# Kernel tuning notes

Hardware: AMD Instinct MI355X
Metric: run time of the kernel (lower is better)

The kernel has to match this reference:

```python
import jax, jax.numpy as jnp
import numpy as np

BS, SEQ, DIM, NH = 4, 2048, 768, 12
DH = DIM // NH  # 64


def setup_inputs() -> dict:
    key = jax.random.key(0)
    ks = jax.random.split(key, 12)
    s = 1.0 / np.sqrt(DIM)
    return {
        "query": jax.random.normal(ks[0], (BS, SEQ, DIM), jnp.float32),
        "key_": jax.random.normal(ks[1], (BS, SEQ, DIM), jnp.float32),
        "value": jax.random.normal(ks[2], (BS, SEQ, DIM), jnp.float32),
        "mask": jax.random.randint(ks[3], (BS, SEQ), 0, 2, jnp.int32),
        "q_w": jax.random.uniform(ks[4], (DIM, DIM), jnp.float32, -s, s),
        "q_b": jax.random.uniform(ks[5], (DIM,), jnp.float32, -s, s),
        "k_w": jax.random.uniform(ks[6], (DIM, DIM), jnp.float32, -s, s),
        "k_b": jax.random.uniform(ks[7], (DIM,), jnp.float32, -s, s),
        "v_w": jax.random.uniform(ks[8], (DIM, DIM), jnp.float32, -s, s),
        "v_b": jax.random.uniform(ks[9], (DIM,), jnp.float32, -s, s),
        "o_w": jax.random.uniform(ks[10], (DIM, DIM), jnp.float32, -s, s),
        "o_b": jax.random.uniform(ks[11], (DIM,), jnp.float32, -s, s),
    }


def reference(query, key_, value, mask, q_w, q_b, k_w, k_b, v_w, v_b, o_w, o_b):
    bs, q_len, _ = query.shape
    # linear projections (torch Linear: x @ W.T + b), split heads -> [b, h, s, d]
    def shape(x):
        return x.reshape(bs, -1, NH, DH).transpose(0, 2, 1, 3)

    q = shape(query @ q_w.T + q_b) / jnp.sqrt(jnp.asarray(DH, query.dtype))
    k = shape(key_ @ k_w.T + k_b)
    v = shape(value @ v_w.T + v_b)

    scores = jnp.einsum("bhqd,bhkd->bhqk", q, k)  # [b, h, q, k]
    neg = jnp.finfo(scores.dtype).min
    pad = (mask == 0)[:, None, None, :]  # [b,1,1,k]
    scores = jnp.where(pad, neg, scores)
    weights = jax.nn.softmax(scores, axis=-1)
    # dropout is identity in eval / deterministic reference
    context = jnp.einsum("bhqk,bhkd->bhqd", weights, v)
    context = context.transpose(0, 2, 1, 3).reshape(bs, q_len, DIM)
    return context @ o_w.T + o_b
```

## Files before the change

### kernel.cpp

```cpp
#include <hip/hip_runtime.h>
#include <hip/hip_bf16.h>

typedef __attribute__((ext_vector_type(8))) short short8;
typedef __attribute__((ext_vector_type(4))) float f32x4;
typedef __attribute__((ext_vector_type(4))) unsigned short u16x4;
typedef __attribute__((ext_vector_type(4))) int int4v;
typedef __attribute__((ext_vector_type(2))) unsigned int u32x2;

#define DEVI static __device__ __forceinline__

constexpr int B_ = 4, S_ = 2048, D_ = 768, NH_ = 12, DH_ = 64;
constexpr int M_ = B_ * S_;
constexpr size_t NX = (size_t)M_ * D_;
constexpr size_t NW = (size_t)D_ * D_;

DEVI unsigned short f2bf(float f) {
  union { float f; unsigned u; } c; c.f = f;
  unsigned u = c.u;
  return (unsigned short)((u + 0x7FFFu + ((u >> 16) & 1u)) >> 16);
}

DEVI unsigned cvtpk_bf16(float lo, float hi) {
  unsigned r;
  asm("v_cvt_pk_bf16_f32 %0, %1, %2" : "=v"(r) : "v"(lo), "v"(hi));
  return r;
}

DEVI float fexp2(float x) {
  float r;
  asm("v_exp_f32 %0, %1" : "=v"(r) : "v"(x));
  return r;
}

DEVI void gload16(const void* g, void* l) {
  __builtin_amdgcn_global_load_lds(
      (const __attribute__((address_space(1))) void*)g,
      (__attribute__((address_space(3))) void*)l, 16, 0, 0);
}

__global__ __launch_bounds__(256) void convert_kernel(
    const float* __restrict__ q, const float* __restrict__ k,
    const float* __restrict__ v, const float* __restrict__ qw_,
    const float* __restrict__ kw_, const float* __restrict__ vw_,
    const float* __restrict__ ow_, const int* __restrict__ smask,
    unsigned short* __restrict__ Xq, unsigned short* __restrict__ Xk,
    unsigned short* __restrict__ Xv, unsigned short* __restrict__ Wc,
    float* __restrict__ dmask) {
  const long bid = blockIdx.x;
  const int tid = threadIdx.x;
  if (bid < 18432) {
    const int seg = (int)(bid / 6144);
    const long i = (bid % 6144) * 256 + tid;
    const float* src = seg == 0 ? q : seg == 1 ? k : v;
    unsigned short* dst = seg == 0 ? Xq : seg == 1 ? Xk : Xv;
    f32x4 vv = *(const f32x4*)(src + i * 4);
    u16x4 o;
    o.x = f2bf(vv.x); o.y = f2bf(vv.y); o.z = f2bf(vv.z); o.w = f2bf(vv.w);
    *(u16x4*)(dst + i * 4) = o;
  } else if (bid < 20736) {
    const long e = ((bid - 18432) * 256 + tid) * 4;
    const int j = (int)(e / (long)NW);
    const float* src = j == 0 ? qw_ : j == 1 ? kw_ : j == 2 ? vw_ : ow_;
    f32x4 vv = *(const f32x4*)(src + (e - (long)j * NW));
    u16x4 o;
    o.x = f2bf(vv.x); o.y = f2bf(vv.y); o.z = f2bf(vv.z); o.w = f2bf(vv.w);
    *(u16x4*)(Wc + e) = o;
  } else {
    const long i = (bid - 20736) * 256 + tid;
    int4v m = *(const int4v*)(smask + i * 4);
    f32x4 o;
    o.x = m.x ? -4.0f : -1e30f; o.y = m.y ? -4.0f : -1e30f;
    o.z = m.z ? -4.0f : -1e30f; o.w = m.w ? -4.0f : -1e30f;
    *(f32x4*)(dmask + i * 4) = o;
  }
}

DEVI void gemm_core(const unsigned short* __restrict__ A,
                    const unsigned short* __restrict__ Bt,
                    unsigned short* As, unsigned short* Bs,
                    int m0, int n0, int tid, f32x4 acc[4][4]) {
  const int w = tid >> 6, l = tid & 63;
  const int wm = w >> 1, wn = w & 1;
  const int lr = l & 15, lg = l >> 4;

  const unsigned short* gA0 = A  + (size_t)(m0 + (tid >> 2)) * 768 + (tid & 3) * 8;
  const unsigned short* gB0 = Bt + (size_t)(n0 + (tid >> 2)) * 768 + (tid & 3) * 8;
  const int wslot = w * 512;

  gload16(gA0, As + wslot);
  gload16(gA0 + (size_t)64 * 768, As + wslot + 2048);
  gload16(gB0, Bs + wslot);
  gload16(gB0 + (size_t)64 * 768, Bs + wslot + 2048);

  int buf = 0;
  for (int k0 = 0; k0 < 768; k0 += 32) {
    if (k0 + 32 < 768) {
      const int nb = (buf ^ 1) * 4096;
      gload16(gA0 + k0 + 32, As + nb + wslot);
      gload16(gA0 + (size_t)64 * 768 + k0 + 32, As + nb + wslot + 2048);
      gload16(gB0 + k0 + 32, Bs + nb + wslot);
      gload16(gB0 + (size_t)64 * 768 + k0 + 32, Bs + nb + wslot + 2048);
      asm volatile("s_waitcnt vmcnt(4)" ::: "memory");
    } else {
      asm volatile("s_waitcnt vmcnt(0)" ::: "memory");
    }
    __builtin_amdgcn_s_barrier();

    const unsigned short* fA = As + buf * 4096 + (size_t)(wm * 64 + lr) * 32 + lg * 8;
    const unsigned short* fB = Bs + buf * 4096 + (size_t)(wn * 64 + lr) * 32 + lg * 8;
    short8 af[4], bf[4];
#pragma unroll
    for (int m = 0; m < 4; m++) af[m] = *(const short8*)(fA + m * 16 * 32);
#pragma unroll
    for (int n = 0; n < 4; n++) bf[n] = *(const short8*)(fB + n * 16 * 32);
    __builtin_amdgcn_s_setprio(1);
#pragma unroll
    for (int m = 0; m < 4; m++)
#pragma unroll
      for (int n = 0; n < 4; n++)
        acc[m][n] = __builtin_amdgcn_mfma_f32_16x16x32_bf16(af[m], bf[n], acc[m][n], 0, 0, 0);
    __builtin_amdgcn_s_setprio(0);
    __builtin_amdgcn_s_barrier();
    buf ^= 1;
  }
}

__global__ __launch_bounds__(256) void qkv_gemm(
    const unsigned short* __restrict__ Xq, const unsigned short* __restrict__ Xk,
    const unsigned short* __restrict__ Xv,
    const unsigned short* __restrict__ Wq, const unsigned short* __restrict__ Wk,
    const unsigned short* __restrict__ Wv,
    const float* __restrict__ bq, const float* __restrict__ bk,
    const float* __restrict__ bv,
    unsigned short* __restrict__ Oq, unsigned short* __restrict__ Ok,
    unsigned short* __restrict__ Vt) {
  __shared__ unsigned short SH[16384];
  const int z = blockIdx.z;
  const unsigned short* A  = (z == 0) ? Xq : (z == 1) ? Xk : Xv;
  const unsigned short* Bt = (z == 0) ? Wq : (z == 1) ? Wk : Wv;
  const float* bias        = (z == 0) ? bq : (z == 1) ? bk : bv;
  const float scale = (z == 0) ? 0.125f * 1.44269504f : 1.0f;

  const int m0 = blockIdx.x * 128, n0 = blockIdx.y * 128;
  f32x4 acc[4][4] = {};
  gemm_core(A, Bt, SH, SH + 8192, m0, n0, threadIdx.x, acc);

  const int tid = threadIdx.x, w = tid >> 6, l = tid & 63;
  const int wm = w >> 1, wn = w & 1, lr = l & 15, lg = l >> 4;
  if (z == 2) {
#pragma unroll
    for (int n = 0; n < 4; n++) {
      const int row = wn * 64 + n * 16 + lr;
      const float bvv = bias[n0 + row];
#pragma unroll
      for (int m = 0; m < 4; m++) {
        const int colb = wm * 64 + m * 16 + lg * 4;
        u16x4 v4;
#pragma unroll
        for (int r = 0; r < 4; r++) v4[r] = f2bf(acc[m][n][r] + bvv);
        *(u16x4*)&SH[row * 128 + (colb ^ ((row & 15) << 3))] = v4;
      }
    }
    __syncthreads();
    const int brow = m0 >> 11;
    const int s0 = m0 & 2047;
    const int u = tid & 15;
#pragma unroll
    for (int p = 0; p < 8; p++) {
      const int row = (tid >> 4) + 16 * p;
      short8 v = *(const short8*)&SH[row * 128 + ((u ^ (row & 15)) << 3)];
      const int ng = n0 + row;
      const int h = ng >> 6, d = ng & 63;
      *(short8*)&Vt[((size_t)(brow * NH_ + h) * DH_ + d) * S_ + s0 + u * 8] = v;
    }
  } else {
    unsigned short* O = (z == 0) ? Oq : Ok;
#pragma unroll
    for (int n = 0; n < 4; n++) {
      const int ng = n0 + wn * 64 + n * 16 + lr;
      const float bvv = bias[ng];
      const int h = ng >> 6, d = ng & 63;
#pragma unroll
      for (int m = 0; m < 4; m++) {
#pragma unroll
        for (int r = 0; r < 4; r++) {
          const int mg = m0 + wm * 64 + m * 16 + lg * 4 + r;
          const int b = mg >> 11, s = mg & 2047;
          O[((size_t)(b * NH_ + h) * S_ + s) * DH_ + d] = f2bf((acc[m][n][r] + bvv) * scale);
        }
      }
    }
  }
}

__global__ __launch_bounds__(256) void out_gemm(
    const unsigned short* __restrict__ A, const unsigned short* __restrict__ Bt,
    const float* __restrict__ bias, float* __restrict__ out) {
  __shared__ unsigned short As[2 * 4096], Bs[2 * 4096];
  const int m0 = blockIdx.x * 128, n0 = blockIdx.y * 128;
  f32x4 acc[4][4] = {};
  gemm_core(A, Bt, As, Bs, m0, n0, threadIdx.x, acc);

  const int tid = threadIdx.x, w = tid >> 6, l = tid & 63;
  const int wm = w >> 1, wn = w & 1, lr = l & 15, lg = l >> 4;
#pragma unroll
  for (int n = 0; n < 4; n++) {
    const int ng = n0 + wn * 64 + n * 16 + lr;
    const float bvv = bias[ng];
#pragma unroll
    for (int m = 0; m < 4; m++) {
#pragma unroll
      for (int r = 0; r < 4; r++) {
        const int mg = m0 + wm * 64 + m * 16 + lg * 4 + r;
        out[(size_t)mg * 768 + ng] = acc[m][n][r] + bvv;
      }
    }
  }
}

__global__ __launch_bounds__(512, 6) void attn_kernel(
    const unsigned short* __restrict__ Qp, const unsigned short* __restrict__ Kp,
    const unsigned short* __restrict__ Vt, const float* __restrict__ maskadd,
    unsigned short* __restrict__ Ctx) {
  __shared__ unsigned short KsA[4096], KsB[4096];
  __shared__ unsigned short VsA[4096], VsB[4096];

  const int id = blockIdx.x;
  const int xcd = id & 7, slot = id >> 3;
  const int bh = xcd + 8 * (slot >> 4);
  const int qt = slot & 15;
  const int b = bh / NH_, h = bh % NH_;
  const int tid = threadIdx.x, w = tid >> 6, l = tid & 63;
  const int lr = l & 15, lg = l >> 4;
  const int rsw = lr & 7;
  const int qw = qt * 128 + w * 16;

  const unsigned short* Qb = Qp + ((size_t)bh * S_ + qw + lr) * DH_ + lg * 8;
  const short8 aq0 = *(const short8*)(Qb);
  const short8 aq1 = *(const short8*)(Qb + 32);

  const int r0 = tid >> 3, c0 = tid & 7;
  const int cg = c0 ^ (r0 & 7);
  const unsigned short* Kg0 = Kp + ((size_t)bh * S_ + r0) * DH_ + cg * 8;
  const unsigned short* Vg0 = Vt + ((size_t)bh * DH_ + r0) * S_ + cg * 8;
  const int wslot = w * 512;

  const float* Mb = maskadd + b * S_ + lg * 4;

  float l_run = 0.f;
  f32x4 ctx[4] = {};

  unsigned short *Krd = KsA, *Vrd = VsA, *Kwr = KsB, *Vwr = VsB;

  gload16(Kg0, KsA + wslot);
  gload16(Vg0, VsA + wslot);
  f32x4 mkc[4];
#pragma unroll
  for (int t = 0; t < 4; t++) mkc[t] = *(const f32x4*)(Mb + 16 * t);
  __syncthreads();

  for (int kt = 0; kt < S_ / 64; kt++) {
    if (kt + 1 < S_ / 64) {
      gload16(Kg0 + (size_t)(kt + 1) * 64 * DH_, Kwr + wslot);
      gload16(Vg0 + (kt + 1) * 64, Vwr + wslot);
    }

    f32x4 sacc[4];
#pragma unroll
    for (int t = 0; t < 4; t++) sacc[t] = mkc[t];
    if (kt + 1 < S_ / 64) {
      const int kvn = (kt + 1) * 64;
#pragma unroll
      for (int t = 0; t < 4; t++) mkc[t] = *(const f32x4*)(Mb + kvn + 16 * t);
    }

    __builtin_amdgcn_s_setprio(1);
#pragma unroll
    for (int t = 0; t < 4; t++) {
      const int row = 16 * t + lr;
      short8 kf0 = *(const short8*)&Krd[row * 64 + ((lg) ^ rsw) * 8];
      short8 kf1 = *(const short8*)&Krd[row * 64 + ((lg + 4) ^ rsw) * 8];
      sacc[t] = __builtin_amdgcn_mfma_f32_16x16x32_bf16(kf0, aq0, sacc[t], 0, 0, 0);
      sacc[t] = __builtin_amdgcn_mfma_f32_16x16x32_bf16(kf1, aq1, sacc[t], 0, 0, 0);
    }
    __builtin_amdgcn_s_setprio(0);

    float ts = 0.f;
#pragma unroll
    for (int t = 0; t < 4; t++)
#pragma unroll
      for (int r = 0; r < 4; r++) {
        const float p = fexp2(sacc[t][r]);
        sacc[t][r] = p; ts += p;
      }
    ts += __shfl_xor(ts, 16);
    ts += __shfl_xor(ts, 32);
    l_run += ts;

    short8 pa[2];
#pragma unroll
    for (int half = 0; half < 2; half++) {
      const int t0 = 2 * half;
      unsigned Ax = cvtpk_bf16(sacc[t0][0], sacc[t0][1]);
      unsigned Ay = cvtpk_bf16(sacc[t0][2], sacc[t0][3]);
      unsigned Bx = cvtpk_bf16(sacc[t0 + 1][0], sacc[t0 + 1][1]);
      unsigned By = cvtpk_bf16(sacc[t0 + 1][2], sacc[t0 + 1][3]);
      asm("v_permlane32_swap_b32 %0, %1" : "+v"(Ax), "+v"(Bx));
      asm("v_permlane16_swap_b32 %0, %1" : "+v"(Ax), "+v"(Bx));
      asm("v_permlane32_swap_b32 %0, %1" : "+v"(Ay), "+v"(By));
      asm("v_permlane16_swap_b32 %0, %1" : "+v"(Ay), "+v"(By));
      union { unsigned u4[4]; short8 s8; } pk;
      pk.u4[0] = Ax; pk.u4[1] = Ay; pk.u4[2] = Bx; pk.u4[3] = By;
      pa[half] = pk.s8;
    }

    __builtin_amdgcn_s_setprio(1);
#pragma unroll
    for (int dt = 0; dt < 4; dt++) {
      const int row = 16 * dt + lr;
      short8 vf0 = *(const short8*)&Vrd[row * 64 + ((lg) ^ rsw) * 8];
      short8 vf1 = *(const short8*)&Vrd[row * 64 + ((lg + 4) ^ rsw) * 8];
      ctx[dt] = __builtin_amdgcn_mfma_f32_16x16x32_bf16(pa[0], vf0, ctx[dt], 0, 0, 0);
      ctx[dt] = __builtin_amdgcn_mfma_f32_16x16x32_bf16(pa[1], vf1, ctx[dt], 0, 0, 0);
    }
    __builtin_amdgcn_s_setprio(0);

    __syncthreads();
    unsigned short* t0p = Krd; Krd = Kwr; Kwr = t0p;
    unsigned short* t1p = Vrd; Vrd = Vwr; Vwr = t1p;
  }

  const float linv = 1.f / l_run;
  float iv[4];
#pragma unroll
  for (int r = 0; r < 4; r++) iv[r] = __shfl(linv, lg * 4 + r, 16);
#pragma unroll
  for (int r = 0; r < 4; r++) {
    const int qg = qw + lg * 4 + r;
#pragma unroll
    for (int dt = 0; dt < 4; dt++) {
      Ctx[((size_t)b * S_ + qg) * D_ + h * DH_ + dt * 16 + lr] =
          f2bf(ctx[dt][r] * iv[r]);
    }
  }
}

extern "C" void kernel_launch(void* const* d_in, const int* in_sizes, int n_in,
                              void* d_out, int out_size, void* d_ws, size_t ws_size,
                              hipStream_t stream) {
  const float* q   = (const float*)d_in[0];
  const float* k   = (const float*)d_in[1];
  const float* v   = (const float*)d_in[2];
  const int* mask  = (const int*)d_in[3];
  const float* q_w = (const float*)d_in[4];
  const float* q_b = (const float*)d_in[5];
  const float* k_w = (const float*)d_in[6];
  const float* k_b = (const float*)d_in[7];
  const float* v_w = (const float*)d_in[8];
  const float* v_b = (const float*)d_in[9];
  const float* o_w = (const float*)d_in[10];
  const float* o_b = (const float*)d_in[11];
  float* out = (float*)d_out;

  unsigned short* ws = (unsigned short*)d_ws;
  unsigned short* Xq = ws;
  unsigned short* Xk = Xq + NX;
  unsigned short* Xv = Xk + NX;
  unsigned short* Wq = Xv + NX;
  unsigned short* Wk = Wq + NW;
  unsigned short* Wv = Wk + NW;
  unsigned short* Wo = Wv + NW;
  unsigned short* Qp = Wo + NW;
  unsigned short* Kp = Qp + NX;
  unsigned short* Vt = Kp + NX;
  float* Ma = (float*)(Vt + NX);
  unsigned short* Ctx = Xq;

  convert_kernel<<<dim3(20744), dim3(256), 0, stream>>>(
      q, k, v, q_w, k_w, v_w, o_w, mask, Xq, Xk, Xv, Wq, Ma);

  qkv_gemm<<<dim3(64, 6, 3), dim3(256), 0, stream>>>(
      Xq, Xk, Xv, Wq, Wk, Wv, q_b, k_b, v_b, Qp, Kp, Vt);

  attn_kernel<<<dim3(768), dim3(512), 0, stream>>>(Qp, Kp, Vt, Ma, Ctx);

  out_gemm<<<dim3(64, 6), dim3(256), 0, stream>>>(Ctx, Wo, o_b, out);
}
```

Baseline: 156.4 us.

## Process two 16-row query blocks per wave to reuse K/V fragments

Each wave in the attention kernel now handles 32 query rows (two 16-row blocks) instead of 16, so each query tile covers 256 rows and the grid halves to 384 blocks. Every K and V fragment read from LDS feeds twice as many MFMAs, and K/V global traffic per query is halved. The cost is more registers per thread: launch bounds drop from 6 to 4 waves, and 384 blocks on 256 CUs may leave work unevenly spread across CUs.

Result: slower. 165.4 us (+5.8%).

```diff
diff --git a/kernel.cpp b/kernel.cpp
--- a/kernel.cpp
+++ b/kernel.cpp
@@ -218,7 +218,7 @@
   }
 }
 
-__global__ __launch_bounds__(512, 6) void attn_kernel(
+__global__ __launch_bounds__(512, 4) void attn_kernel(
     const unsigned short* __restrict__ Qp, const unsigned short* __restrict__ Kp,
     const unsigned short* __restrict__ Vt, const float* __restrict__ maskadd,
     unsigned short* __restrict__ Ctx) {
@@ -227,17 +227,21 @@
 
   const int id = blockIdx.x;
   const int xcd = id & 7, slot = id >> 3;
-  const int bh = xcd + 8 * (slot >> 4);
-  const int qt = slot & 15;
+  const int bh = xcd + 8 * (slot >> 3);
+  const int qt = slot & 7;
   const int b = bh / NH_, h = bh % NH_;
   const int tid = threadIdx.x, w = tid >> 6, l = tid & 63;
   const int lr = l & 15, lg = l >> 4;
   const int rsw = lr & 7;
-  const int qw = qt * 128 + w * 16;
-
-  const unsigned short* Qb = Qp + ((size_t)bh * S_ + qw + lr) * DH_ + lg * 8;
-  const short8 aq0 = *(const short8*)(Qb);
-  const short8 aq1 = *(const short8*)(Qb + 32);
+  const int qw = qt * 256 + w * 32;
+
+  short8 aq[2][2];
+#pragma unroll
+  for (int qb = 0; qb < 2; qb++)
+#pragma unroll
+    for (int ks = 0; ks < 2; ks++)
+      aq[qb][ks] = *(const short8*)&Qp[((size_t)bh * S_ + qw + qb * 16 + lr) * DH_ +
+                                       lg * 8 + ks * 32];
 
   const int r0 = tid >> 3, c0 = tid & 7;
   const int cg = c0 ^ (r0 & 7);
@@ -247,8 +251,8 @@
 
   const float* Mb = maskadd + b * S_ + lg * 4;
 
-  float l_run = 0.f;
-  f32x4 ctx[4] = {};
+  float l_run[2] = {0.f, 0.f};
+  f32x4 ctx[2][4] = {};
 
   unsigned short *Krd = KsA, *Vrd = VsA, *Kwr = KsB, *Vwr = VsB;
 
@@ -265,53 +269,56 @@
       gload16(Vg0 + (kt + 1) * 64, Vwr + wslot);
     }
 
-    f32x4 sacc[4];
-#pragma unroll
-    for (int t = 0; t < 4; t++) sacc[t] = mkc[t];
-    if (kt + 1 < S_ / 64) {
-      const int kvn = (kt + 1) * 64;
-#pragma unroll
-      for (int t = 0; t < 4; t++) mkc[t] = *(const f32x4*)(Mb + kvn + 16 * t);
-    }
-
+    f32x4 sacc[2][4];
     __builtin_amdgcn_s_setprio(1);
 #pragma unroll
     for (int t = 0; t < 4; t++) {
       const int row = 16 * t + lr;
       short8 kf0 = *(const short8*)&Krd[row * 64 + ((lg) ^ rsw) * 8];
       short8 kf1 = *(const short8*)&Krd[row * 64 + ((lg + 4) ^ rsw) * 8];
-      sacc[t] = __builtin_amdgcn_mfma_f32_16x16x32_bf16(kf0, aq0, sacc[t], 0, 0, 0);
-      sacc[t] = __builtin_amdgcn_mfma_f32_16x16x32_bf16(kf1, aq1, sacc[t], 0, 0, 0);
+      sacc[0][t] = __builtin_amdgcn_mfma_f32_16x16x32_bf16(kf0, aq[0][0], mkc[t], 0, 0, 0);
+      sacc[0][t] = __builtin_amdgcn_mfma_f32_16x16x32_bf16(kf1, aq[0][1], sacc[0][t], 0, 0, 0);
+      sacc[1][t] = __builtin_amdgcn_mfma_f32_16x16x32_bf16(kf0, aq[1][0], mkc[t], 0, 0, 0);
+      sacc[1][t] = __builtin_amdgcn_mfma_f32_16x16x32_bf16(kf1, aq[1][1], sacc[1][t], 0, 0, 0);
     }
     __builtin_amdgcn_s_setprio(0);
 
-    float ts = 0.f;
-#pragma unroll
-    for (int t = 0; t < 4; t++)
-#pragma unroll
-      for (int r = 0; r < 4; r++) {
-        const float p = fexp2(sacc[t][r]);
-        sacc[t][r] = p; ts += p;
+    if (kt + 1 < S_ / 64) {
+      const int kvn = (kt + 1) * 64;
+#pragma unroll
+      for (int t = 0; t < 4; t++) mkc[t] = *(const f32x4*)(Mb + kvn + 16 * t);
+    }
+
+    short8 pa[2][2];
+#pragma unroll
+    for (int qb = 0; qb < 2; qb++) {
+      float ts = 0.f;
+#pragma unroll
+      for (int t = 0; t < 4; t++)
+#pragma unroll
+        for (int r = 0; r < 4; r++) {
+          const float p = fexp2(sacc[qb][t][r]);
+          sacc[qb][t][r] = p; ts += p;
+        }
+      ts += __shfl_xor(ts, 16);
+      ts += __shfl_xor(ts, 32);
+      l_run[qb] += ts;
+
+#pragma unroll
+      for (int half = 0; half < 2; half++) {
+        const int t0 = 2 * half;
+        unsigned Ax = cvtpk_bf16(sacc[qb][t0][0], sacc[qb][t0][1]);
+        unsigned Ay = cvtpk_bf16(sacc[qb][t0][2], sacc[qb][t0][3]);
+        unsigned Bx = cvtpk_bf16(sacc[qb][t0 + 1][0], sacc[qb][t0 + 1][1]);
+        unsigned By = cvtpk_bf16(sacc[qb][t0 + 1][2], sacc[qb][t0 + 1][3]);
+        asm("v_permlane32_swap_b32 %0, %1" : "+v"(Ax), "+v"(Bx));
+        asm("v_permlane16_swap_b32 %0, %1" : "+v"(Ax), "+v"(Bx));
+        asm("v_permlane32_swap_b32 %0, %1" : "+v"(Ay), "+v"(By));
+        asm("v_permlane16_swap_b32 %0, %1" : "+v"(Ay), "+v"(By));
+        union { unsigned u4[4]; short8 s8; } pk;
+        pk.u4[0] = Ax; pk.u4[1] = Ay; pk.u4[2] = Bx; pk.u4[3] = By;
+        pa[qb][half] = pk.s8;
       }
-    ts += __shfl_xor(ts, 16);
-    ts += __shfl_xor(ts, 32);
-    l_run += ts;
-
-    short8 pa[2];
-#pragma unroll
-    for (int half = 0; half < 2; half++) {
-      const int t0 = 2 * half;
-      unsigned Ax = cvtpk_bf16(sacc[t0][0], sacc[t0][1]);
-      unsigned Ay = cvtpk_bf16(sacc[t0][2], sacc[t0][3]);
-      unsigned Bx = cvtpk_bf16(sacc[t0 + 1][0], sacc[t0 + 1][1]);
-      unsigned By = cvtpk_bf16(sacc[t0 + 1][2], sacc[t0 + 1][3]);
-      asm("v_permlane32_swap_b32 %0, %1" : "+v"(Ax), "+v"(Bx));
-      asm("v_permlane16_swap_b32 %0, %1" : "+v"(Ax), "+v"(Bx));
-      asm("v_permlane32_swap_b32 %0, %1" : "+v"(Ay), "+v"(By));
-      asm("v_permlane16_swap_b32 %0, %1" : "+v"(Ay), "+v"(By));
-      union { unsigned u4[4]; short8 s8; } pk;
-      pk.u4[0] = Ax; pk.u4[1] = Ay; pk.u4[2] = Bx; pk.u4[3] = By;
-      pa[half] = pk.s8;
     }
 
     __builtin_amdgcn_s_setprio(1);
@@ -320,8 +327,10 @@
       const int row = 16 * dt + lr;
       short8 vf0 = *(const short8*)&Vrd[row * 64 + ((lg) ^ rsw) * 8];
       short8 vf1 = *(const short8*)&Vrd[row * 64 + ((lg + 4) ^ rsw) * 8];
-      ctx[dt] = __builtin_amdgcn_mfma_f32_16x16x32_bf16(pa[0], vf0, ctx[dt], 0, 0, 0);
-      ctx[dt] = __builtin_amdgcn_mfma_f32_16x16x32_bf16(pa[1], vf1, ctx[dt], 0, 0, 0);
+      ctx[0][dt] = __builtin_amdgcn_mfma_f32_16x16x32_bf16(pa[0][0], vf0, ctx[0][dt], 0, 0, 0);
+      ctx[0][dt] = __builtin_amdgcn_mfma_f32_16x16x32_bf16(pa[0][1], vf1, ctx[0][dt], 0, 0, 0);
+      ctx[1][dt] = __builtin_amdgcn_mfma_f32_16x16x32_bf16(pa[1][0], vf0, ctx[1][dt], 0, 0, 0);
+      ctx[1][dt] = __builtin_amdgcn_mfma_f32_16x16x32_bf16(pa[1][1], vf1, ctx[1][dt], 0, 0, 0);
     }
     __builtin_amdgcn_s_setprio(0);
 
@@ -330,17 +339,20 @@
     unsigned short* t1p = Vrd; Vrd = Vwr; Vwr = t1p;
   }
 
-  const float linv = 1.f / l_run;
-  float iv[4];
-#pragma unroll
-  for (int r = 0; r < 4; r++) iv[r] = __shfl(linv, lg * 4 + r, 16);
-#pragma unroll
-  for (int r = 0; r < 4; r++) {
-    const int qg = qw + lg * 4 + r;
-#pragma unroll
-    for (int dt = 0; dt < 4; dt++) {
-      Ctx[((size_t)b * S_ + qg) * D_ + h * DH_ + dt * 16 + lr] =
-          f2bf(ctx[dt][r] * iv[r]);
+#pragma unroll
+  for (int qb = 0; qb < 2; qb++) {
+    const float linv = 1.f / l_run[qb];
+    float iv[4];
+#pragma unroll
+    for (int r = 0; r < 4; r++) iv[r] = __shfl(linv, lg * 4 + r, 16);
+#pragma unroll
+    for (int r = 0; r < 4; r++) {
+      const int qg = qw + qb * 16 + lg * 4 + r;
+#pragma unroll
+      for (int dt = 0; dt < 4; dt++) {
+        Ctx[((size_t)b * S_ + qg) * D_ + h * DH_ + dt * 16 + lr] =
+            f2bf(ctx[qb][dt][r] * iv[r]);
+      }
     }
   }
 }
@@ -382,7 +394,7 @@
   qkv_gemm<<<dim3(64, 6, 3), dim3(256), 0, stream>>>(
       Xq, Xk, Xv, Wq, Wk, Wv, q_b, k_b, v_b, Qp, Kp, Vt);
 
-  attn_kernel<<<dim3(768), dim3(512), 0, stream>>>(Qp, Kp, Vt, Ma, Ctx);
+  attn_kernel<<<dim3(384), dim3(512), 0, stream>>>(Qp, Kp, Vt, Ma, Ctx);
 
   out_gemm<<<dim3(64, 6), dim3(256), 0, stream>>>(Ctx, Wo, o_b, out);
 }
```
